# Kernel optimization log

Hardware: AMD Instinct MI355X
Metric: run time of the kernel (lower is better)

The kernel has to match this reference:

```python
import jax, jax.numpy as jnp
import numpy as np

S = 14
L_COORD = 5.0
L_NOOBJ = 0.5
EPS = 1e-20


def _corners(box):
    # box: (..., 5) with [x, y, w, h, c]; convert center/size -> corner coords (per torch code)
    xc = box[..., 0] / S
    yc = box[..., 1] / S
    x1 = xc - 0.5 * box[..., 2]
    y1 = yc - 0.5 * box[..., 3]
    x2 = xc + 0.5 * box[..., 2]
    y2 = yc + 0.5 * box[..., 3]
    return x1, y1, x2, y2


def _pairwise_diag_iou(bt, bp):
    # bt, bp: (..., 5). Torch builds an NxM IoU matrix and takes the diagonal;
    # the diagonal is just the elementwise (row-wise) IoU, computed here directly.
    tx1, ty1, tx2, ty2 = _corners(bt)
    px1, py1, px2, py2 = _corners(bp)
    iw = jnp.maximum(jnp.minimum(tx2, px2) - jnp.maximum(tx1, px1), 0.0)
    ih = jnp.maximum(jnp.minimum(ty2, py2) - jnp.maximum(ty1, py1), 0.0)
    inter = iw * ih
    area_t = (tx2 - tx1) * (ty2 - ty1)
    area_p = (px2 - px1) * (py2 - py1)
    return inter / (area_t + area_p - inter)


def yolo_loss(pred, tgt):
    N = pred.shape[0]
    dt = pred.dtype

    obj = (tgt[..., 4] + tgt[..., 9]) > 0            # (N,S,S) cells containing an object
    objf = obj.astype(dt)
    noobjf = 1.0 - objf

    # --- no-object loss: confidences (ch 4 and 9) of no-object cells ---
    no_object_loss = jnp.sum(
        noobjf * ((pred[..., 4] - tgt[..., 4]) ** 2 + (pred[..., 9] - tgt[..., 9]) ** 2)
    )

    # --- class loss over object cells ---
    class_loss = jnp.sum(objf * jnp.sum((pred[..., 10:30] - tgt[..., 10:30]) ** 2, axis=-1))

    # --- per-cell box pairs ---
    bp = pred[..., :10].reshape(pred.shape[:3] + (2, 5))   # (N,S,S,2,5)
    bt = tgt[..., :10].reshape(tgt.shape[:3] + (2, 5))

    iou = jax.lax.stop_gradient(_pairwise_diag_iou(bt, bp))  # (N,S,S,2); detached in torch

    # Responsible-box selection, faithfully replicating the torch stride-2 trick:
    # a[::2] = iou0 > iou1 ; a[1::2] = float(a[::2]) <= iou1
    iou0, iou1 = iou[..., 0], iou[..., 1]
    a0 = iou0 > iou1
    a1 = a0.astype(dt) <= iou1
    sel = jnp.stack([a0, a1], axis=-1).astype(dt)          # (N,S,S,2)
    w = objf[..., None] * sel                              # response weight per box

    # --- containing-object confidence loss (target = detached IoU) ---
    contain_loss = jnp.sum(w * (bp[..., 4] - iou) ** 2)

    dx = bp[..., 0] - bt[..., 0]
    dy = bp[..., 1] - bt[..., 1]
    dsw = jnp.sqrt(bp[..., 2] + EPS) - jnp.sqrt(bt[..., 2] + EPS)
    dsh = jnp.sqrt(bp[..., 3] + EPS) - jnp.sqrt(bt[..., 3] + EPS)
    regression_loss = jnp.sum(w * (dx ** 2 + dy ** 2 + dsw ** 2 + dsh ** 2))

    total = (L_COORD * regression_loss + contain_loss
             + L_NOOBJ * no_object_loss + class_loss) / N
    return total


def setup_inputs() -> dict:
    key = jax.random.key(0)
    k1, k2, k3 = jax.random.split(key, 3)
    N = 4096
    pred = jax.random.uniform(k1, (N, S, S, 30), dtype=jnp.float32)
    tgt = jax.random.uniform(k2, (N, S, S, 30), dtype=jnp.float32)
    obj_cell = (jax.random.uniform(k3, (N, S, S)) < 0.05).astype(jnp.float32)
    tgt = tgt.at[..., 4].multiply(obj_cell)
    tgt = tgt.at[..., 9].multiply(obj_cell)
    return {"pred_tensor": pred, "target_tensor": tgt}


def reference(pred_tensor, target_tensor):
    return yolo_loss(pred_tensor, target_tensor)
```

## Files before the change

kernel.cpp:

```cpp
#include <hip/hip_runtime.h>

namespace {
constexpr int   S_GRID   = 14;
constexpr int   CH       = 30;
constexpr float L_COORD  = 5.0f;
constexpr float L_NOOBJ  = 0.5f;
constexpr float BOX_EPS  = 1e-20f;
constexpr int   BLOCK    = 256;
constexpr int   NSLOT    = 256;
constexpr int   SLOT_STRIDE = 16;
}

__global__ __launch_bounds__(BLOCK) void yolo_main_kernel(
    const float* __restrict__ pred,
    const float* __restrict__ tgt,
    float* __restrict__ partial)
{
    __shared__ float wsum[BLOCK / 64];

    const int tid  = threadIdx.x;
    const size_t cell = (size_t)blockIdx.x * BLOCK + tid;

    const float* p = pred + cell * CH;
    const float* t = tgt  + cell * CH;

    float pv[CH], tv[CH];
    #pragma unroll
    for (int j = 0; j < CH / 2; ++j) {
        float2 a = reinterpret_cast<const float2*>(p)[j];
        pv[2 * j] = a.x; pv[2 * j + 1] = a.y;
        float2 b = reinterpret_cast<const float2*>(t)[j];
        tv[2 * j] = b.x; tv[2 * j + 1] = b.y;
    }

    const float objf   = ((tv[4] + tv[9]) > 0.0f) ? 1.0f : 0.0f;
    const float noobjf = 1.0f - objf;

    const float d4 = pv[4] - tv[4];
    const float d9 = pv[9] - tv[9];
    const float no_obj = noobjf * (d4 * d4 + d9 * d9);

    float cls = 0.0f;
    #pragma unroll
    for (int j = 10; j < CH; ++j) {
        const float d = pv[j] - tv[j];
        cls += d * d;
    }
    cls *= objf;

    float iou[2];
    constexpr float invS = 1.0f / (float)S_GRID;
    #pragma unroll
    for (int b = 0; b < 2; ++b) {
        const float* bp = pv + 5 * b;
        const float* bt = tv + 5 * b;
        const float txc = bt[0] * invS, tyc = bt[1] * invS;
        const float tx1 = txc - 0.5f * bt[2], tx2 = txc + 0.5f * bt[2];
        const float ty1 = tyc - 0.5f * bt[3], ty2 = tyc + 0.5f * bt[3];
        const float pxc = bp[0] * invS, pyc = bp[1] * invS;
        const float px1 = pxc - 0.5f * bp[2], px2 = pxc + 0.5f * bp[2];
        const float py1 = pyc - 0.5f * bp[3], py2 = pyc + 0.5f * bp[3];
        const float iw = fmaxf(fminf(tx2, px2) - fmaxf(tx1, px1), 0.0f);
        const float ih = fmaxf(fminf(ty2, py2) - fmaxf(ty1, py1), 0.0f);
        const float inter  = iw * ih;
        const float area_t = (tx2 - tx1) * (ty2 - ty1);
        const float area_p = (px2 - px1) * (py2 - py1);
        iou[b] = inter / (area_t + area_p - inter);
    }

    const bool  a0   = iou[0] > iou[1];
    const bool  a1   = (a0 ? 1.0f : 0.0f) <= iou[1];
    const float sel0 = a0 ? 1.0f : 0.0f;
    const float sel1 = a1 ? 1.0f : 0.0f;

    float contain = 0.0f, regr = 0.0f;
    #pragma unroll
    for (int b = 0; b < 2; ++b) {
        const float w  = objf * (b == 0 ? sel0 : sel1);
        const float* bp = pv + 5 * b;
        const float* bt = tv + 5 * b;
        const float dc = bp[4] - iou[b];
        contain += w * dc * dc;
        const float dx  = bp[0] - bt[0];
        const float dy  = bp[1] - bt[1];
        const float dsw = sqrtf(bp[2] + BOX_EPS) - sqrtf(bt[2] + BOX_EPS);
        const float dsh = sqrtf(bp[3] + BOX_EPS) - sqrtf(bt[3] + BOX_EPS);
        regr += w * (dx * dx + dy * dy + dsw * dsw + dsh * dsh);
    }

    float acc = L_COORD * regr + contain + L_NOOBJ * no_obj + cls;

    #pragma unroll
    for (int off = 32; off > 0; off >>= 1)
        acc += __shfl_down(acc, off, 64);
    const int lane = tid & 63;
    const int wid  = tid >> 6;
    if (lane == 0) wsum[wid] = acc;
    __syncthreads();
    if (tid == 0) {
        const float s = (wsum[0] + wsum[1]) + (wsum[2] + wsum[3]);
        atomicAdd(&partial[(blockIdx.x & (NSLOT - 1)) * SLOT_STRIDE], s);
    }
}

__global__ __launch_bounds__(NSLOT) void yolo_finalize_kernel(
    const float* __restrict__ partial,
    float* __restrict__ out,
    float inv_n)
{
    __shared__ float wsum[NSLOT / 64];
    const int tid = threadIdx.x;
    float v = partial[tid * SLOT_STRIDE];
    #pragma unroll
    for (int off = 32; off > 0; off >>= 1)
        v += __shfl_down(v, off, 64);
    const int lane = tid & 63;
    const int wid  = tid >> 6;
    if (lane == 0) wsum[wid] = v;
    __syncthreads();
    if (tid == 0)
        out[0] = ((wsum[0] + wsum[1]) + (wsum[2] + wsum[3])) * inv_n;
}

extern "C" void kernel_launch(void* const* d_in, const int* in_sizes, int n_in,
                              void* d_out, int out_size, void* d_ws, size_t ws_size,
                              hipStream_t stream) {
    const float* pred = (const float*)d_in[0];
    const float* tgt  = (const float*)d_in[1];
    float* out     = (float*)d_out;
    float* partial = (float*)d_ws;

    const int ncells  = in_sizes[0] / CH;
    const int n_batch = ncells / (S_GRID * S_GRID);
    const int grid    = ncells / BLOCK;

    hipMemsetAsync(partial, 0, NSLOT * SLOT_STRIDE * sizeof(float), stream);
    yolo_main_kernel<<<grid, BLOCK, 0, stream>>>(pred, tgt, partial);
    yolo_finalize_kernel<<<1, NSLOT, 0, stream>>>(partial, out,
                                                  1.0f / (float)n_batch);
}
```

Before: 210.8 us.

## Stage coalesced wave tiles through LDS with persistent grid and register prefetch

Each wave now loads a 64-cell tile of pred and tgt with fully coalesced float2 loads, stages it in per-wave shared memory, and then has each lane read its own 30-float row from LDS. A fixed persistent grid of 512 blocks loops over tiles, and the next tile is prefetched into registers while the current one is computed. This replaces the strided per-thread 120-byte loads that had poor coalescing. In exchange it uses many more registers and about 61 KB of LDS per block, which may limit occupancy. It also adds a shared-memory round trip that can hit bank conflicts because the per-lane rows use a stride of 30 floats.

```diff
diff --git a/kernel.cpp b/kernel.cpp
--- a/kernel.cpp
+++ b/kernel.cpp
@@ -7,32 +7,19 @@
 constexpr float L_NOOBJ  = 0.5f;
 constexpr float BOX_EPS  = 1e-20f;
 constexpr int   BLOCK    = 256;
+constexpr int   WAVES_PB = BLOCK / 64;
+constexpr int   WTILE    = 64;
+constexpr int   WFLOATS  = WTILE * CH;
+constexpr int   NCHUNK   = WFLOATS / 2 / 64;
+constexpr int   GRID     = 512;
+constexpr int   NWAVES   = GRID * WAVES_PB;
 constexpr int   NSLOT    = 256;
 constexpr int   SLOT_STRIDE = 16;
 }
 
-__global__ __launch_bounds__(BLOCK) void yolo_main_kernel(
-    const float* __restrict__ pred,
-    const float* __restrict__ tgt,
-    float* __restrict__ partial)
+__device__ __forceinline__ float cell_loss(const float* __restrict__ pv,
+                                           const float* __restrict__ tv)
 {
-    __shared__ float wsum[BLOCK / 64];
-
-    const int tid  = threadIdx.x;
-    const size_t cell = (size_t)blockIdx.x * BLOCK + tid;
-
-    const float* p = pred + cell * CH;
-    const float* t = tgt  + cell * CH;
-
-    float pv[CH], tv[CH];
-    #pragma unroll
-    for (int j = 0; j < CH / 2; ++j) {
-        float2 a = reinterpret_cast<const float2*>(p)[j];
-        pv[2 * j] = a.x; pv[2 * j + 1] = a.y;
-        float2 b = reinterpret_cast<const float2*>(t)[j];
-        tv[2 * j] = b.x; tv[2 * j + 1] = b.y;
-    }
-
     const float objf   = ((tv[4] + tv[9]) > 0.0f) ? 1.0f : 0.0f;
     const float noobjf = 1.0f - objf;
 
@@ -88,13 +75,78 @@
         regr += w * (dx * dx + dy * dy + dsw * dsw + dsh * dsh);
     }
 
-    float acc = L_COORD * regr + contain + L_NOOBJ * no_obj + cls;
+    return L_COORD * regr + contain + L_NOOBJ * no_obj + cls;
+}
+
+__global__ __launch_bounds__(BLOCK, 2) void yolo_main_kernel(
+    const float* __restrict__ pred,
+    const float* __restrict__ tgt,
+    float* __restrict__ partial,
+    int ntiles)
+{
+    __shared__ float sbuf[WAVES_PB][2 * WFLOATS];
+    __shared__ float wsum[WAVES_PB];
+
+    const int tid  = threadIdx.x;
+    const int lane = tid & 63;
+    const int wid  = tid >> 6;
+    const int wglob = blockIdx.x * WAVES_PB + wid;
+
+    float2* wp2 = reinterpret_cast<float2*>(sbuf[wid]);
+    float2* wt2 = reinterpret_cast<float2*>(sbuf[wid] + WFLOATS);
+
+    float2 bp[NCHUNK], bt[NCHUNK];
+    float  acc = 0.0f;
+
+    int t = wglob;
+    if (t < ntiles) {
+        const float2* gp = reinterpret_cast<const float2*>(pred) + (size_t)t * (WFLOATS / 2);
+        const float2* gt = reinterpret_cast<const float2*>(tgt)  + (size_t)t * (WFLOATS / 2);
+        #pragma unroll
+        for (int j = 0; j < NCHUNK; ++j) {
+            bp[j] = gp[j * 64 + lane];
+            bt[j] = gt[j * 64 + lane];
+        }
+    }
+
+    while (t < ntiles) {
+        #pragma unroll
+        for (int j = 0; j < NCHUNK; ++j) {
+            wp2[j * 64 + lane] = bp[j];
+            wt2[j * 64 + lane] = bt[j];
+        }
+
+        const int tn = t + NWAVES;
+        if (tn < ntiles) {
+            const float2* gp = reinterpret_cast<const float2*>(pred) + (size_t)tn * (WFLOATS / 2);
+            const float2* gt = reinterpret_cast<const float2*>(tgt)  + (size_t)tn * (WFLOATS / 2);
+            #pragma unroll
+            for (int j = 0; j < NCHUNK; ++j) {
+                bp[j] = gp[j * 64 + lane];
+                bt[j] = gt[j * 64 + lane];
+            }
+        }
+
+        float pv[CH], tv[CH];
+        {
+            const float2* rowp = reinterpret_cast<const float2*>(sbuf[wid] + lane * CH);
+            const float2* rowt = reinterpret_cast<const float2*>(sbuf[wid] + WFLOATS + lane * CH);
+            #pragma unroll
+            for (int j = 0; j < CH / 2; ++j) {
+                const float2 a = rowp[j];
+                pv[2 * j] = a.x; pv[2 * j + 1] = a.y;
+                const float2 b = rowt[j];
+                tv[2 * j] = b.x; tv[2 * j + 1] = b.y;
+            }
+        }
+        acc += cell_loss(pv, tv);
+
+        t = tn;
+    }
 
     #pragma unroll
     for (int off = 32; off > 0; off >>= 1)
         acc += __shfl_down(acc, off, 64);
-    const int lane = tid & 63;
-    const int wid  = tid >> 6;
     if (lane == 0) wsum[wid] = acc;
     __syncthreads();
     if (tid == 0) {
@@ -132,10 +184,10 @@
 
     const int ncells  = in_sizes[0] / CH;
     const int n_batch = ncells / (S_GRID * S_GRID);
-    const int grid    = ncells / BLOCK;
+    const int ntiles  = ncells / WTILE;
 
     hipMemsetAsync(partial, 0, NSLOT * SLOT_STRIDE * sizeof(float), stream);
-    yolo_main_kernel<<<grid, BLOCK, 0, stream>>>(pred, tgt, partial);
+    yolo_main_kernel<<<GRID, BLOCK, 0, stream>>>(pred, tgt, partial, ntiles);
     yolo_finalize_kernel<<<1, NSLOT, 0, stream>>>(partial, out,
                                                   1.0f / (float)n_batch);
 }
```

After: 206.2 us. 2.2% less time.
